# Performance work log

Measured on AMD Instinct MI355X. Metric: run time of the kernel, lower is better.

The kernel has to match this reference:

```python
import jax, jax.numpy as jnp
import numpy as np

N = 30000      # num nodes (cells)
E = 480000     # num edges (avg degree 16)
D_IN = 1000    # input_dim (genes)
H = 8          # nheads
F_H = 32       # hidden_dim per head
D_EMB = 64     # embedding_dim
NEG_SLOPE = 0.2


def setup_inputs() -> dict:
    key = jax.random.key(0)
    ks = jax.random.split(key, 12)
    glorot = lambda k, shape, fan: (jax.random.normal(k, shape, jnp.float32)
                                    * (1.0 / np.sqrt(fan)))
    return {
        "x": jax.random.normal(ks[0], (N, D_IN), jnp.float32),
        "edge_index": jax.random.randint(ks[1], (2, E), 0, N),
        "edge_weight": jax.random.uniform(ks[2], (E,), jnp.float32),
        # GATConv params
        "W": glorot(ks[3], (D_IN, H * F_H), D_IN),
        "att_src": glorot(ks[4], (H, F_H), F_H),
        "att_dst": glorot(ks[5], (H, F_H), F_H),
        "bias_gat": jnp.zeros((H * F_H,), jnp.float32),
        # embedding Linear
        "emb_W": glorot(ks[6], (H * F_H, D_EMB), H * F_H),
        "emb_b": jnp.zeros((D_EMB,), jnp.float32),
        # decoder MLP
        "dec_W1": glorot(ks[7], (D_EMB, F_H), D_EMB),
        "dec_b1": jnp.zeros((F_H,), jnp.float32),
        "dec_W2": glorot(ks[8], (F_H, D_IN), F_H),
        "dec_b2": jnp.zeros((D_IN,), jnp.float32),
    }


def _gat_conv(x, edge_index, W, att_src, att_dst, bias):
    n = x.shape[0]
    h = (x @ W).reshape(n, H, F_H)                    # [N,H,F]
    a_s = jnp.einsum('nhf,hf->nh', h, att_src)        # [N,H]
    a_d = jnp.einsum('nhf,hf->nh', h, att_dst)        # [N,H]
    # add self loops (PyG default add_self_loops=True)
    loops = jnp.arange(n)
    src = jnp.concatenate([edge_index[0], loops])     # [E+N]
    dst = jnp.concatenate([edge_index[1], loops])     # [E+N]
    logits = jax.nn.leaky_relu(a_s[src] + a_d[dst], NEG_SLOPE)  # [E+N,H]
    # segment softmax over incoming edges of each destination node
    m = jax.ops.segment_max(logits, dst, num_segments=n)        # [N,H]
    p = jnp.exp(logits - m[dst])
    denom = jax.ops.segment_sum(p, dst, num_segments=n)         # [N,H]
    alpha = p / denom[dst]                                      # [E+N,H]
    msg = h[src] * alpha[:, :, None]                            # [E+N,H,F]
    out = jax.ops.segment_sum(msg, dst, num_segments=n)         # [N,H,F]
    return out.reshape(n, H * F_H) + bias


def reference(x, edge_index, edge_weight, W, att_src, att_dst, bias_gat,
              emb_W, emb_b, dec_W1, dec_b1, dec_W2, dec_b2):
    # edge_weight is accepted but unused: PyG GATConv with edge_dim=None has
    # no edge-feature pathway.
    h = jax.nn.relu(_gat_conv(x, edge_index, W, att_src, att_dst, bias_gat))
    z = h @ emb_W + emb_b                               # [N, D_EMB]
    d = jax.nn.relu(z @ dec_W1 + dec_b1)                # [N, F_H]
    recon = d @ dec_W2 + dec_b2                         # [N, D_IN]
    return recon, z
```

## Files before the change

kernel.cpp:

```cpp
#include <hip/hip_runtime.h>
#include <hip/hip_bf16.h>

#define N_NODES 30000
#define N_EDGES 480000
#define D_IN    1000
#define KPAD    1024
#define NHEAD   8
#define F_HID   32
#define D_EMB   64
#define NEG_SLOPE 0.2f
#define MAXDEG  64

typedef __attribute__((ext_vector_type(4))) float  f32x4;
typedef __attribute__((ext_vector_type(8))) __bf16 bf16x8;
typedef __attribute__((ext_vector_type(4))) __bf16 bf16x4;

#define WT_TOT    (256*KPAD + D_EMB*256 + F_HID*D_EMB + D_IN*F_HID)
#define WT_BLOCKS ((WT_TOT + 255) / 256)
#define WA_BLOCKS (16 * KPAD / 256)
#define SC_CHUNK  4068
#define SC_BLOCKS (118 * 8)

__global__ __launch_bounds__(256) void cvt_w(
    const float* __restrict__ W, const float* __restrict__ emb_W,
    const float* __restrict__ d1, const float* __restrict__ d2,
    const float* __restrict__ att_src, const float* __restrict__ att_dst,
    __bf16* __restrict__ WbT, __bf16* __restrict__ embT,
    __bf16* __restrict__ d1T, __bf16* __restrict__ d2T,
    __bf16* __restrict__ WaT,
    const int* __restrict__ eidx, int* __restrict__ cnt,
    int* __restrict__ slots)
{
    int b = blockIdx.x;
    if (b < WT_BLOCKS) {
        int i = b * 256 + threadIdx.x;
        if (i < 256 * KPAD) {
            int n = i >> 10, k = i & 1023;
            WbT[i] = (k < D_IN) ? (__bf16)W[(size_t)k * 256 + n] : (__bf16)0.0f;
            return;
        }
        i -= 256 * KPAD;
        if (i < D_EMB * 256) {
            int n = i >> 8, k = i & 255;
            embT[i] = (__bf16)emb_W[(size_t)k * D_EMB + n];
            return;
        }
        i -= D_EMB * 256;
        if (i < F_HID * D_EMB) {
            int n = i >> 6, k = i & 63;
            d1T[i] = (__bf16)d1[(size_t)k * F_HID + n];
            return;
        }
        i -= F_HID * D_EMB;
        if (i < D_IN * F_HID) {
            int n = i >> 5, k = i & 31;
            d2T[i] = (__bf16)d2[(size_t)k * D_IN + n];
        }
        return;
    }
    b -= WT_BLOCKS;
    if (b < WA_BLOCKS) {
        int i = b * 256 + threadIdx.x;
        int j = i >> 10, k = i & 1023;
        float s = 0.f;
        if (k < D_IN) {
            const float* av = (j < 8 ? att_src : att_dst) + (j & 7) * F_HID;
            const float* wr = W + (size_t)k * 256 + (j & 7) * F_HID;
            #pragma unroll
            for (int f = 0; f < F_HID; f++) s += wr[f] * av[f];
        }
        WaT[i] = (__bf16)s;
        return;
    }
    b -= WA_BLOCKS;
    {
        const int shard = blockIdx.x & 7;
        const int chunk = b >> 3;
        int e0 = chunk * SC_CHUNK;
        int e1 = e0 + SC_CHUNK; if (e1 > N_EDGES) e1 = N_EDGES;
        for (int e = e0 + (int)threadIdx.x; e < e1; e += 256) {
            int d = eidx[N_EDGES + e];
            if (((d >> 4) & 7) == shard) {
                int slot = atomicAdd(&cnt[d], 1);
                slots[d * MAXDEG + slot] = eidx[e];
            }
        }
    }
}

__device__ __forceinline__ void stage_tile(
    __bf16* lds, const __bf16* __restrict__ g, int base, int maxr,
    int K, int k0, int rows, int w, int lane, int stride)
{
    const int rsub = lane >> 2;
    const int c    = lane & 3;
    for (int off = w * 1024; off < rows * 64; off += stride) {
        int r  = (off >> 6) + rsub;
        int gr = base + r; gr = gr > maxr ? maxr : gr;
        int chunk = c ^ (r & 3);
        const __bf16* gp = g + (size_t)gr * K + k0 + chunk * 8;
        __builtin_amdgcn_global_load_lds(
            (const __attribute__((address_space(1))) void*)gp,
            (__attribute__((address_space(3))) void*)((char*)lds + off),
            16, 0, 0);
    }
}

#define GEMM1_BLOCKS ((N_NODES + 63) / 64)

__device__ __forceinline__ void xload8(const float* __restrict__ xrow, int cb,
                                       f32x4& u0, f32x4& u1)
{
    if (cb < D_IN) {
        const f32x4* p = (const f32x4*)(xrow + cb);
        u0 = p[0]; u1 = p[1];
    } else {
        u0 = (f32x4){0.f, 0.f, 0.f, 0.f};
        u1 = (f32x4){0.f, 0.f, 0.f, 0.f};
    }
}

__device__ __forceinline__ bf16x8 cvt8(const f32x4& u0, const f32x4& u1)
{
    bf16x8 o;
    o[0] = (__bf16)u0.x; o[1] = (__bf16)u0.y; o[2] = (__bf16)u0.z; o[3] = (__bf16)u0.w;
    o[4] = (__bf16)u1.x; o[5] = (__bf16)u1.y; o[6] = (__bf16)u1.z; o[7] = (__bf16)u1.w;
    return o;
}

__global__ __launch_bounds__(512, 4) void gemm1_fused(
    const float* __restrict__ x, const __bf16* __restrict__ WbT,
    const __bf16* __restrict__ WaT, __bf16* __restrict__ hb,
    float* __restrict__ a_s, float* __restrict__ a_d, int M)
{
    __shared__ __align__(16) __bf16 As[2][64 * 32];
    __shared__ __align__(16) __bf16 Bs[2][256 * 32];

    const int tid  = threadIdx.x;
    const int w    = tid >> 6, lane = tid & 63;
    const int wm   = w >> 2,   wn   = w & 3;
    const int quad = lane >> 4, l16 = lane & 15;
    const int bm   = blockIdx.x * 64;

    const bool astage = (tid < 256);
    const int r0   = tid >> 2;
    const int cpos = tid & 3;
    const int cxor = (cpos ^ (r0 & 3)) << 3;
    int grow = bm + r0; if (grow > M - 1) grow = M - 1;
    const float* xrow = x + (size_t)grow * D_IN;

    const int brsub = lane >> 2;
    const int bc    = lane & 3;

    f32x4 acc[2][4];
    #pragma unroll
    for (int i = 0; i < 2; i++)
        #pragma unroll
        for (int j = 0; j < 4; j++)
            acc[i][j] = (f32x4){0.f, 0.f, 0.f, 0.f};
    f32x4 accA[2];
    #pragma unroll
    for (int i = 0; i < 2; i++) accA[i] = (f32x4){0.f, 0.f, 0.f, 0.f};

    const bool att = (wn == 0);
    const __bf16* warow = WaT + (size_t)l16 * KPAD + quad * 8;

    auto stageB = [&](int buf, int k0) {
        #pragma unroll
        for (int off = 0; off < 16384; off += 8192) {
            int o2 = off + w * 1024;
            int r = (o2 >> 6) + brsub;
            int chunk = bc ^ (r & 3);
            const __bf16* gp = WbT + (size_t)r * KPAD + k0 + chunk * 8;
            __builtin_amdgcn_global_load_lds(
                (const __attribute__((address_space(1))) void*)gp,
                (__attribute__((address_space(3))) void*)((char*)&Bs[buf][0] + o2),
                16, 0, 0);
        }
    };

    auto compute = [&](int buf, const bf16x8& attfrag) {
        bf16x8 af[2], bfr[4];
        #pragma unroll
        for (int mt = 0; mt < 2; mt++) {
            int r = wm * 32 + mt * 16 + l16;
            af[mt] = *(const bf16x8*)&As[buf][r * 32 + (quad ^ (r & 3)) * 8];
        }
        #pragma unroll
        for (int nt = 0; nt < 4; nt++) {
            int r = wn * 64 + nt * 16 + l16;
            bfr[nt] = *(const bf16x8*)&Bs[buf][r * 32 + (quad ^ (r & 3)) * 8];
        }
        #pragma unroll
        for (int mt = 0; mt < 2; mt++)
            #pragma unroll
            for (int nt = 0; nt < 4; nt++)
                acc[mt][nt] = __builtin_amdgcn_mfma_f32_16x16x32_bf16(
                    af[mt], bfr[nt], acc[mt][nt], 0, 0, 0);
        if (att) {
            #pragma unroll
            for (int mt = 0; mt < 2; mt++)
                accA[mt] = __builtin_amdgcn_mfma_f32_16x16x32_bf16(
                    af[mt], attfrag, accA[mt], 0, 0, 0);
        }
    };

    f32x4 xa0, xa1, xb0, xb1;
    bf16x8 attEv = {}, attOd = {};

    if (astage) {
        xload8(xrow, 0 + cxor, xa0, xa1);
        xload8(xrow, 32 + cxor, xb0, xb1);
    }
    if (att) attEv = *(const bf16x8*)(warow + 0);
    if (astage) *(bf16x8*)&As[0][r0 * 32 + cpos * 8] = cvt8(xa0, xa1);
    stageB(0, 0);
    __syncthreads();

    for (int k0 = 0; k0 < KPAD; k0 += 64) {
        if (astage) {
            xload8(xrow, (k0 + 64) + cxor, xa0, xa1);
            *(bf16x8*)&As[1][r0 * 32 + cpos * 8] = cvt8(xb0, xb1);
        }
        if (att) attOd = *(const bf16x8*)(warow + k0 + 32);
        stageB(1, k0 + 32);
        compute(0, attEv);
        __syncthreads();

        if (k0 + 64 < KPAD) {
            if (astage) {
                xload8(xrow, (k0 + 96) + cxor, xb0, xb1);
                *(bf16x8*)&As[0][r0 * 32 + cpos * 8] = cvt8(xa0, xa1);
            }
            if (att) attEv = *(const bf16x8*)(warow + k0 + 64);
            stageB(0, k0 + 64);
        }
        compute(1, attOd);
        __syncthreads();
    }

    #pragma unroll
    for (int nt = 0; nt < 4; nt++) {
        int col = wn * 64 + nt * 16 + l16;
        #pragma unroll
        for (int mt = 0; mt < 2; mt++) {
            int row0 = bm + wm * 32 + mt * 16 + quad * 4;
            #pragma unroll
            for (int rr = 0; rr < 4; rr++) {
                int row = row0 + rr;
                if (row < M)
                    hb[(size_t)row * 256 + col] = (__bf16)acc[mt][nt][rr];
            }
        }
    }
    if (att) {
        #pragma unroll
        for (int mt = 0; mt < 2; mt++) {
            int row0 = bm + wm * 32 + mt * 16 + quad * 4;
            #pragma unroll
            for (int rr = 0; rr < 4; rr++) {
                int row = row0 + rr;
                if (row < M) {
                    float v = accA[mt][rr];
                    if (l16 < 8) a_s[row * NHEAD + l16] = v;
                    else         a_d[row * NHEAD + (l16 - 8)] = v;
                }
            }
        }
    }
}

__device__ __forceinline__ float leaky(float x) {
    return x > 0.f ? x : NEG_SLOPE * x;
}

__global__ __launch_bounds__(256) void gat_aggregate(
    const __bf16* __restrict__ hb, const float* __restrict__ a_s,
    const float* __restrict__ a_d, const int* __restrict__ cnt,
    const int* __restrict__ slots, const float* __restrict__ bias,
    __bf16* __restrict__ hgatb)
{
    const int wid  = threadIdx.x >> 6;
    const int lane = threadIdx.x & 63;
    const int n = blockIdx.x * 4 + wid;
    if (n >= N_NODES) return;

    const int hh = lane >> 3;
    const int fo = (lane & 7) * 4;
    const int base = n * MAXDEG;
    const int c = cnt[n];
    const float adn = a_d[n * NHEAD + hh];

    float p = __expf(leaky(a_s[n * NHEAD + hh] + adn));
    float denom = p;
    f32x4 acc;
    {
        bf16x4 hv = *(const bf16x4*)(hb + (size_t)n * 256 + hh * F_HID + fo);
        acc.x = p * (float)hv[0]; acc.y = p * (float)hv[1];
        acc.z = p * (float)hv[2]; acc.w = p * (float)hv[3];
    }
    int e = 0;
    for (; e + 4 <= c; e += 4) {
        const int4 ss = *(const int4*)(slots + base + e);
        int s0 = ss.x, s1 = ss.y, s2 = ss.z, s3 = ss.w;
        float l0 = a_s[s0 * NHEAD + hh], l1 = a_s[s1 * NHEAD + hh];
        float l2 = a_s[s2 * NHEAD + hh], l3 = a_s[s3 * NHEAD + hh];
        bf16x4 h0 = *(const bf16x4*)(hb + (size_t)s0 * 256 + hh * F_HID + fo);
        bf16x4 h1 = *(const bf16x4*)(hb + (size_t)s1 * 256 + hh * F_HID + fo);
        bf16x4 h2 = *(const bf16x4*)(hb + (size_t)s2 * 256 + hh * F_HID + fo);
        bf16x4 h3 = *(const bf16x4*)(hb + (size_t)s3 * 256 + hh * F_HID + fo);
        float p0 = __expf(leaky(l0 + adn)), p1 = __expf(leaky(l1 + adn));
        float p2 = __expf(leaky(l2 + adn)), p3 = __expf(leaky(l3 + adn));
        denom += (p0 + p1) + (p2 + p3);
        acc.x += p0*(float)h0[0] + p1*(float)h1[0] + p2*(float)h2[0] + p3*(float)h3[0];
        acc.y += p0*(float)h0[1] + p1*(float)h1[1] + p2*(float)h2[1] + p3*(float)h3[1];
        acc.z += p0*(float)h0[2] + p1*(float)h1[2] + p2*(float)h2[2] + p3*(float)h3[2];
        acc.w += p0*(float)h0[3] + p1*(float)h1[3] + p2*(float)h2[3] + p3*(float)h3[3];
    }
    for (; e < c; e++) {
        int s = slots[base + e];
        float pe = __expf(leaky(a_s[s * NHEAD + hh] + adn));
        denom += pe;
        bf16x4 hv = *(const bf16x4*)(hb + (size_t)s * 256 + hh * F_HID + fo);
        acc.x += pe * (float)hv[0]; acc.y += pe * (float)hv[1];
        acc.z += pe * (float)hv[2]; acc.w += pe * (float)hv[3];
    }
    float inv = 1.0f / denom;
    f32x4 bv = *(const f32x4*)(bias + lane * 4);
    float o0 = acc.x * inv + bv.x, o1 = acc.y * inv + bv.y;
    float o2 = acc.z * inv + bv.z, o3 = acc.w * inv + bv.w;
    o0 = o0 > 0.f ? o0 : 0.f;
    o1 = o1 > 0.f ? o1 : 0.f;
    o2 = o2 > 0.f ? o2 : 0.f;
    o3 = o3 > 0.f ? o3 : 0.f;
    bf16x4 ob;
    ob[0] = (__bf16)o0; ob[1] = (__bf16)o1; ob[2] = (__bf16)o2; ob[3] = (__bf16)o3;
    *(bf16x4*)(hgatb + (size_t)n * 256 + lane * 4) = ob;
}

__global__ __launch_bounds__(256) void gemm_zdr(
    const __bf16* __restrict__ hgatb, const __bf16* __restrict__ embT,
    const __bf16* __restrict__ d1T, const __bf16* __restrict__ d2T,
    const float* __restrict__ emb_b, const float* __restrict__ dec_b1,
    const float* __restrict__ dec_b2, float* __restrict__ z,
    float* __restrict__ recon, int M)
{
    __shared__ __align__(16) __bf16 smem[10240];
    __bf16* As  = smem;
    __bf16* Bs  = smem + 2048;
    __bf16* zS  = smem + 4096;
    __bf16* Bs2 = smem + 8192;

    const int tid  = threadIdx.x;
    const int w    = tid >> 6, lane = tid & 63;
    const int wm   = w >> 1,   wn   = w & 1;
    const int quad = lane >> 4, l16 = lane & 15;
    const int bm = blockIdx.x * 64;

    stage_tile(Bs2,        d1T, 0, 31, 64, 0,  32, w, lane, 4096);
    stage_tile(Bs2 + 1024, d1T, 0, 31, 64, 32, 32, w, lane, 4096);

    f32x4 acc[2][2];
    #pragma unroll
    for (int i = 0; i < 2; i++) { acc[i][0] = (f32x4){0,0,0,0}; acc[i][1] = (f32x4){0,0,0,0}; }

    for (int k0 = 0; k0 < 256; k0 += 32) {
        stage_tile(As, hgatb, bm, M - 1, 256, k0, 64, w, lane, 4096);
        stage_tile(Bs, embT,  0,  D_EMB - 1, 256, k0, 64, w, lane, 4096);
        __syncthreads();
        bf16x8 af[2], bfr[2];
        #pragma unroll
        for (int mt = 0; mt < 2; mt++) {
            int r = wm * 32 + mt * 16 + l16;
            af[mt] = *(const bf16x8*)&As[r * 32 + (quad ^ (r & 3)) * 8];
        }
        #pragma unroll
        for (int nt = 0; nt < 2; nt++) {
            int r = wn * 32 + nt * 16 + l16;
            bfr[nt] = *(const bf16x8*)&Bs[r * 32 + (quad ^ (r & 3)) * 8];
        }
        #pragma unroll
        for (int mt = 0; mt < 2; mt++)
            #pragma unroll
            for (int nt = 0; nt < 2; nt++)
                acc[mt][nt] = __builtin_amdgcn_mfma_f32_16x16x32_bf16(
                    af[mt], bfr[nt], acc[mt][nt], 0, 0, 0);
        __syncthreads();
    }

    #pragma unroll
    for (int nt = 0; nt < 2; nt++) {
        int col = wn * 32 + nt * 16 + l16;
        float bv = emb_b[col];
        int t = col >> 5, cch = (col >> 3) & 3, j = col & 7;
        #pragma unroll
        for (int mt = 0; mt < 2; mt++) {
            int rl0 = wm * 32 + mt * 16 + quad * 4;
            #pragma unroll
            for (int rr = 0; rr < 4; rr++) {
                int rl = rl0 + rr;
                int row = bm + rl;
                float v = acc[mt][nt][rr] + bv;
                if (row < M) z[(size_t)row * D_EMB + col] = v;
                zS[t * 2048 + rl * 32 + (cch ^ (rl & 3)) * 8 + j] = (__bf16)v;
            }
        }
    }
    __syncthreads();

    f32x4 accd[2];
    accd[0] = (f32x4){0,0,0,0}; accd[1] = (f32x4){0,0,0,0};
    #pragma unroll
    for (int t = 0; t < 2; t++) {
        bf16x8 af[2], bfr;
        #pragma unroll
        for (int mt = 0; mt < 2; mt++) {
            int r = wm * 32 + mt * 16 + l16;
            af[mt] = *(const bf16x8*)&zS[t * 2048 + r * 32 + (quad ^ (r & 3)) * 8];
        }
        {
            int r = wn * 16 + l16;
            bfr = *(const bf16x8*)&Bs2[t * 1024 + r * 32 + (quad ^ (r & 3)) * 8];
        }
        #pragma unroll
        for (int mt = 0; mt < 2; mt++)
            accd[mt] = __builtin_amdgcn_mfma_f32_16x16x32_bf16(af[mt], bfr, accd[mt], 0, 0, 0);
    }
    {
        int col = wn * 16 + l16;
        float bv = dec_b1[col];
        int cc = col >> 3, j = col & 7;
        #pragma unroll
        for (int mt = 0; mt < 2; mt++) {
            int rl0 = wm * 32 + mt * 16 + quad * 4;
            #pragma unroll
            for (int rr = 0; rr < 4; rr++) {
                int rl = rl0 + rr;
                float v = accd[mt][rr] + bv;
                v = v > 0.f ? v : 0.f;
                As[rl * 32 + (cc ^ (rl & 3)) * 8 + j] = (__bf16)v;
            }
        }
    }
    __syncthreads();

    bf16x8 daf[2];
    #pragma unroll
    for (int mt = 0; mt < 2; mt++) {
        int r = wm * 32 + mt * 16 + l16;
        daf[mt] = *(const bf16x8*)&As[r * 32 + (quad ^ (r & 3)) * 8];
    }
    for (int tt = wn; tt < 63; tt += 2) {
        int crow = tt * 16 + l16;
        if (crow > D_IN - 1) crow = D_IN - 1;
        bf16x8 bfr = *(const bf16x8*)&d2T[(size_t)crow * 32 + quad * 8];
        f32x4 a[2];
        #pragma unroll
        for (int mt = 0; mt < 2; mt++) {
            a[mt] = (f32x4){0.f, 0.f, 0.f, 0.f};
            a[mt] = __builtin_amdgcn_mfma_f32_16x16x32_bf16(bfr, daf[mt], a[mt], 0, 0, 0);
        }
        int col0 = tt * 16 + quad * 4;
        if (col0 + 3 < D_IN) {
            f32x4 bv = *(const f32x4*)&dec_b2[col0];
            #pragma unroll
            for (int mt = 0; mt < 2; mt++) {
                int row = bm + wm * 32 + mt * 16 + l16;
                if (row < M) {
                    f32x4 o;
                    o.x = a[mt].x + bv.x; o.y = a[mt].y + bv.y;
                    o.z = a[mt].z + bv.z; o.w = a[mt].w + bv.w;
                    *(f32x4*)&recon[(size_t)row * D_IN + col0] = o;
                }
            }
        }
    }
}

extern "C" void kernel_launch(void* const* d_in, const int* in_sizes, int n_in,
                              void* d_out, int out_size, void* d_ws, size_t ws_size,
                              hipStream_t stream)
{
    const float* x        = (const float*)d_in[0];
    const int*   eidx     = (const int*)  d_in[1];
    const float* W        = (const float*)d_in[3];
    const float* att_src  = (const float*)d_in[4];
    const float* att_dst  = (const float*)d_in[5];
    const float* bias_gat = (const float*)d_in[6];
    const float* emb_W    = (const float*)d_in[7];
    const float* emb_b    = (const float*)d_in[8];
    const float* dec_W1   = (const float*)d_in[9];
    const float* dec_b1   = (const float*)d_in[10];
    const float* dec_W2   = (const float*)d_in[11];
    const float* dec_b2   = (const float*)d_in[12];

    float* out   = (float*)d_out;
    float* recon = out;
    float* z     = out + (size_t)N_NODES * D_IN;

    char* ws = (char*)d_ws;
    size_t o = 0;
    auto alloc = [&](size_t bytes) { char* p = ws + o; o = (o + bytes + 255) & ~(size_t)255; return p; };
    __bf16* hb      = (__bf16*)alloc((size_t)N_NODES * 256 * 2);
    __bf16* WbT     = (__bf16*)alloc((size_t)256 * KPAD * 2);
    __bf16* embT    = (__bf16*)alloc((size_t)D_EMB * 256 * 2);
    __bf16* d1T     = (__bf16*)alloc((size_t)F_HID * D_EMB * 2);
    __bf16* d2T     = (__bf16*)alloc((size_t)D_IN * F_HID * 2);
    __bf16* WaT     = (__bf16*)alloc((size_t)16 * KPAD * 2);
    __bf16* hgatb   = (__bf16*)alloc((size_t)N_NODES * 256 * 2);
    float*  a_s     = (float*) alloc((size_t)N_NODES * NHEAD * 4);
    float*  a_d     = (float*) alloc((size_t)N_NODES * NHEAD * 4);
    int*    slots   = (int*)   alloc((size_t)N_NODES * MAXDEG * 4);
    int*    cnt     = (int*)   alloc((size_t)N_NODES * 4);

    hipMemsetAsync(cnt, 0, (size_t)N_NODES * 4, stream);

    cvt_w<<<WT_BLOCKS + WA_BLOCKS + SC_BLOCKS, 256, 0, stream>>>(
        W, emb_W, dec_W1, dec_W2, att_src, att_dst,
        WbT, embT, d1T, d2T, WaT, eidx, cnt, slots);

    gemm1_fused<<<GEMM1_BLOCKS, 512, 0, stream>>>(
        x, WbT, WaT, hb, a_s, a_d, N_NODES);

    gat_aggregate<<<N_NODES / 4, 256, 0, stream>>>(
        hb, a_s, a_d, cnt, slots, bias_gat, hgatb);

    gemm_zdr<<<(N_NODES + 63) / 64, 256, 0, stream>>>(
        hgatb, embT, d1T, d2T, emb_b, dec_b1, dec_b2, z, recon, N_NODES);
}
```

Before: 376.1 us.

## Drop LDS staging in gemm1; load W fragments directly from global per wave

Rewrites the first GEMM so each wave owns 16 rows and all 256 output columns. A and B fragments are loaded straight from global memory into registers, so the LDS double-buffering and barriers are gone. The aim is to remove shared-memory traffic and synchronisation overhead. In exchange every wave re-reads the full W matrix from global/L2 with no reuse across waves, and the 16 accumulators plus 16 B fragments raise register pressure.

```diff
diff --git a/kernel.cpp b/kernel.cpp
--- a/kernel.cpp
+++ b/kernel.cpp
@@ -108,18 +108,6 @@
 
 #define GEMM1_BLOCKS ((N_NODES + 63) / 64)
 
-__device__ __forceinline__ void xload8(const float* __restrict__ xrow, int cb,
-                                       f32x4& u0, f32x4& u1)
-{
-    if (cb < D_IN) {
-        const f32x4* p = (const f32x4*)(xrow + cb);
-        u0 = p[0]; u1 = p[1];
-    } else {
-        u0 = (f32x4){0.f, 0.f, 0.f, 0.f};
-        u1 = (f32x4){0.f, 0.f, 0.f, 0.f};
-    }
-}
-
 __device__ __forceinline__ bf16x8 cvt8(const f32x4& u0, const f32x4& u1)
 {
     bf16x8 o;
@@ -128,144 +116,75 @@
     return o;
 }
 
-__global__ __launch_bounds__(512, 4) void gemm1_fused(
+__global__ __launch_bounds__(256) void gemm1_fused(
     const float* __restrict__ x, const __bf16* __restrict__ WbT,
     const __bf16* __restrict__ WaT, __bf16* __restrict__ hb,
     float* __restrict__ a_s, float* __restrict__ a_d, int M)
 {
-    __shared__ __align__(16) __bf16 As[2][64 * 32];
-    __shared__ __align__(16) __bf16 Bs[2][256 * 32];
-
     const int tid  = threadIdx.x;
-    const int w    = tid >> 6, lane = tid & 63;
-    const int wm   = w >> 2,   wn   = w & 3;
+    const int wv   = tid >> 6, lane = tid & 63;
     const int quad = lane >> 4, l16 = lane & 15;
     const int bm   = blockIdx.x * 64;
 
-    const bool astage = (tid < 256);
-    const int r0   = tid >> 2;
-    const int cpos = tid & 3;
-    const int cxor = (cpos ^ (r0 & 3)) << 3;
-    int grow = bm + r0; if (grow > M - 1) grow = M - 1;
-    const float* xrow = x + (size_t)grow * D_IN;
-
-    const int brsub = lane >> 2;
-    const int bc    = lane & 3;
-
-    f32x4 acc[2][4];
-    #pragma unroll
-    for (int i = 0; i < 2; i++)
-        #pragma unroll
-        for (int j = 0; j < 4; j++)
-            acc[i][j] = (f32x4){0.f, 0.f, 0.f, 0.f};
-    f32x4 accA[2];
-    #pragma unroll
-    for (int i = 0; i < 2; i++) accA[i] = (f32x4){0.f, 0.f, 0.f, 0.f};
-
-    const bool att = (wn == 0);
-    const __bf16* warow = WaT + (size_t)l16 * KPAD + quad * 8;
-
-    auto stageB = [&](int buf, int k0) {
-        #pragma unroll
-        for (int off = 0; off < 16384; off += 8192) {
-            int o2 = off + w * 1024;
-            int r = (o2 >> 6) + brsub;
-            int chunk = bc ^ (r & 3);
-            const __bf16* gp = WbT + (size_t)r * KPAD + k0 + chunk * 8;
-            __builtin_amdgcn_global_load_lds(
-                (const __attribute__((address_space(1))) void*)gp,
-                (__attribute__((address_space(3))) void*)((char*)&Bs[buf][0] + o2),
-                16, 0, 0);
+    int arow = bm + wv * 16 + l16; if (arow > M - 1) arow = M - 1;
+    const float* xrow = x + (size_t)arow * D_IN;
+    const int koff = quad * 8;
+
+    f32x4 acc[16];
+    #pragma unroll
+    for (int i = 0; i < 16; i++) acc[i] = (f32x4){0.f, 0.f, 0.f, 0.f};
+    f32x4 accA = (f32x4){0.f, 0.f, 0.f, 0.f};
+
+    const __bf16* wb   = WbT + (size_t)l16 * KPAD + koff;
+    const __bf16* wa   = WaT + (size_t)l16 * KPAD + koff;
+
+    auto loadx = [&](int k0, f32x4& u0, f32x4& u1) {
+        int kk = k0 + koff;
+        if (kk < D_IN) {
+            const f32x4* p = (const f32x4*)(xrow + kk);
+            u0 = p[0]; u1 = p[1];
+        } else {
+            u0 = (f32x4){0.f, 0.f, 0.f, 0.f};
+            u1 = (f32x4){0.f, 0.f, 0.f, 0.f};
         }
     };
 
-    auto compute = [&](int buf, const bf16x8& attfrag) {
-        bf16x8 af[2], bfr[4];
-        #pragma unroll
-        for (int mt = 0; mt < 2; mt++) {
-            int r = wm * 32 + mt * 16 + l16;
-            af[mt] = *(const bf16x8*)&As[buf][r * 32 + (quad ^ (r & 3)) * 8];
-        }
-        #pragma unroll
-        for (int nt = 0; nt < 4; nt++) {
-            int r = wn * 64 + nt * 16 + l16;
-            bfr[nt] = *(const bf16x8*)&Bs[buf][r * 32 + (quad ^ (r & 3)) * 8];
-        }
-        #pragma unroll
-        for (int mt = 0; mt < 2; mt++)
-            #pragma unroll
-            for (int nt = 0; nt < 4; nt++)
-                acc[mt][nt] = __builtin_amdgcn_mfma_f32_16x16x32_bf16(
-                    af[mt], bfr[nt], acc[mt][nt], 0, 0, 0);
-        if (att) {
-            #pragma unroll
-            for (int mt = 0; mt < 2; mt++)
-                accA[mt] = __builtin_amdgcn_mfma_f32_16x16x32_bf16(
-                    af[mt], attfrag, accA[mt], 0, 0, 0);
-        }
-    };
-
-    f32x4 xa0, xa1, xb0, xb1;
-    bf16x8 attEv = {}, attOd = {};
-
-    if (astage) {
-        xload8(xrow, 0 + cxor, xa0, xa1);
-        xload8(xrow, 32 + cxor, xb0, xb1);
-    }
-    if (att) attEv = *(const bf16x8*)(warow + 0);
-    if (astage) *(bf16x8*)&As[0][r0 * 32 + cpos * 8] = cvt8(xa0, xa1);
-    stageB(0, 0);
-    __syncthreads();
-
-    for (int k0 = 0; k0 < KPAD; k0 += 64) {
-        if (astage) {
-            xload8(xrow, (k0 + 64) + cxor, xa0, xa1);
-            *(bf16x8*)&As[1][r0 * 32 + cpos * 8] = cvt8(xb0, xb1);
-        }
-        if (att) attOd = *(const bf16x8*)(warow + k0 + 32);
-        stageB(1, k0 + 32);
-        compute(0, attEv);
-        __syncthreads();
-
-        if (k0 + 64 < KPAD) {
-            if (astage) {
-                xload8(xrow, (k0 + 96) + cxor, xb0, xb1);
-                *(bf16x8*)&As[0][r0 * 32 + cpos * 8] = cvt8(xa0, xa1);
-            }
-            if (att) attEv = *(const bf16x8*)(warow + k0 + 64);
-            stageB(0, k0 + 64);
-        }
-        compute(1, attOd);
-        __syncthreads();
-    }
-
-    #pragma unroll
-    for (int nt = 0; nt < 4; nt++) {
-        int col = wn * 64 + nt * 16 + l16;
-        #pragma unroll
-        for (int mt = 0; mt < 2; mt++) {
-            int row0 = bm + wm * 32 + mt * 16 + quad * 4;
-            #pragma unroll
-            for (int rr = 0; rr < 4; rr++) {
-                int row = row0 + rr;
-                if (row < M)
-                    hb[(size_t)row * 256 + col] = (__bf16)acc[mt][nt][rr];
-            }
-        }
-    }
-    if (att) {
-        #pragma unroll
-        for (int mt = 0; mt < 2; mt++) {
-            int row0 = bm + wm * 32 + mt * 16 + quad * 4;
-            #pragma unroll
-            for (int rr = 0; rr < 4; rr++) {
-                int row = row0 + rr;
-                if (row < M) {
-                    float v = accA[mt][rr];
-                    if (l16 < 8) a_s[row * NHEAD + l16] = v;
-                    else         a_d[row * NHEAD + (l16 - 8)] = v;
-                }
-            }
+    f32x4 xc0, xc1, xn0, xn1;
+    loadx(0, xc0, xc1);
+
+    for (int k0 = 0; k0 < KPAD; k0 += 32) {
+        loadx(k0 + 32, xn0, xn1);
+        bf16x8 bfr[16];
+        #pragma unroll
+        for (int nt = 0; nt < 16; nt++)
+            bfr[nt] = *(const bf16x8*)(wb + (size_t)nt * 16 * KPAD + k0);
+        bf16x8 attf = *(const bf16x8*)(wa + k0);
+        bf16x8 af = cvt8(xc0, xc1);
+        #pragma unroll
+        for (int nt = 0; nt < 16; nt++)
+            acc[nt] = __builtin_amdgcn_mfma_f32_16x16x32_bf16(af, bfr[nt], acc[nt], 0, 0, 0);
+        accA = __builtin_amdgcn_mfma_f32_16x16x32_bf16(af, attf, accA, 0, 0, 0);
+        xc0 = xn0; xc1 = xn1;
+    }
+
+    const int row0 = bm + wv * 16 + quad * 4;
+    #pragma unroll
+    for (int nt = 0; nt < 16; nt++) {
+        int col = nt * 16 + l16;
+        #pragma unroll
+        for (int rr = 0; rr < 4; rr++) {
+            int row = row0 + rr;
+            if (row < M)
+                hb[(size_t)row * 256 + col] = (__bf16)acc[nt][rr];
+        }
+    }
+    #pragma unroll
+    for (int rr = 0; rr < 4; rr++) {
+        int row = row0 + rr;
+        if (row < M) {
+            float v = accA[rr];
+            if (l16 < 8) a_s[row * NHEAD + l16] = v;
+            else         a_d[row * NHEAD + (l16 - 8)] = v;
         }
     }
 }
@@ -519,7 +438,7 @@
         W, emb_W, dec_W1, dec_W2, att_src, att_dst,
         WbT, embT, d1T, d2T, WaT, eidx, cnt, slots);
 
-    gemm1_fused<<<GEMM1_BLOCKS, 512, 0, stream>>>(
+    gemm1_fused<<<GEMM1_BLOCKS, 256, 0, stream>>>(
         x, WbT, WaT, hb, a_s, a_d, N_NODES);
 
     gat_aggregate<<<N_NODES / 4, 256, 0, stream>>>(
```

Measured after the change: 457.9 us. 21.7% more time.

## Shrink GEMM1 block to four waves each computing a full 64x64 tile

Applied to the files above, without the earlier changes.

The main x@W GEMM kernel moves from 512 threads (8 waves, 2x4 wave grid, 32x64 per wave) to 256 threads (4 waves, each 64 rows by 64 cols). Every thread now stages A, which removes the idle half of threads during x loading, and B staging goes through a shared stage_tile helper. Each wave reuses more of its A and B fragments per MFMA, but it holds twice as many accumulators, which raises register pressure and may lower occupancy and latency hiding. The attention-logit MFMA path now runs only on wave 0, covering four m-tiles.

```diff
diff --git a/kernel.cpp b/kernel.cpp
--- a/kernel.cpp
+++ b/kernel.cpp
@@ -128,7 +128,7 @@
     return o;
 }
 
-__global__ __launch_bounds__(512, 4) void gemm1_fused(
+__global__ __launch_bounds__(256, 2) void gemm1_fused(
     const float* __restrict__ x, const __bf16* __restrict__ WbT,
     const __bf16* __restrict__ WaT, __bf16* __restrict__ hb,
     float* __restrict__ a_s, float* __restrict__ a_d, int M)
@@ -137,69 +137,54 @@
     __shared__ __align__(16) __bf16 Bs[2][256 * 32];
 
     const int tid  = threadIdx.x;
-    const int w    = tid >> 6, lane = tid & 63;
-    const int wm   = w >> 2,   wn   = w & 3;
+    const int wv   = tid >> 6, lane = tid & 63;
     const int quad = lane >> 4, l16 = lane & 15;
     const int bm   = blockIdx.x * 64;
 
-    const bool astage = (tid < 256);
     const int r0   = tid >> 2;
     const int cpos = tid & 3;
     const int cxor = (cpos ^ (r0 & 3)) << 3;
     int grow = bm + r0; if (grow > M - 1) grow = M - 1;
     const float* xrow = x + (size_t)grow * D_IN;
 
-    const int brsub = lane >> 2;
-    const int bc    = lane & 3;
-
-    f32x4 acc[2][4];
-    #pragma unroll
-    for (int i = 0; i < 2; i++)
+    f32x4 acc[4][4];
+    #pragma unroll
+    for (int i = 0; i < 4; i++)
         #pragma unroll
         for (int j = 0; j < 4; j++)
             acc[i][j] = (f32x4){0.f, 0.f, 0.f, 0.f};
-    f32x4 accA[2];
-    #pragma unroll
-    for (int i = 0; i < 2; i++) accA[i] = (f32x4){0.f, 0.f, 0.f, 0.f};
-
-    const bool att = (wn == 0);
+    f32x4 accA[4];
+    #pragma unroll
+    for (int i = 0; i < 4; i++) accA[i] = (f32x4){0.f, 0.f, 0.f, 0.f};
+
+    const bool att = (wv == 0);
     const __bf16* warow = WaT + (size_t)l16 * KPAD + quad * 8;
 
     auto stageB = [&](int buf, int k0) {
-        #pragma unroll
-        for (int off = 0; off < 16384; off += 8192) {
-            int o2 = off + w * 1024;
-            int r = (o2 >> 6) + brsub;
-            int chunk = bc ^ (r & 3);
-            const __bf16* gp = WbT + (size_t)r * KPAD + k0 + chunk * 8;
-            __builtin_amdgcn_global_load_lds(
-                (const __attribute__((address_space(1))) void*)gp,
-                (__attribute__((address_space(3))) void*)((char*)&Bs[buf][0] + o2),
-                16, 0, 0);
-        }
+        stage_tile(&Bs[buf][0], WbT, 0, 255, KPAD, k0, 256, wv, lane, 4096);
     };
 
     auto compute = [&](int buf, const bf16x8& attfrag) {
-        bf16x8 af[2], bfr[4];
-        #pragma unroll
-        for (int mt = 0; mt < 2; mt++) {
-            int r = wm * 32 + mt * 16 + l16;
+        bf16x8 af[4], bfr[4];
+        #pragma unroll
+        for (int mt = 0; mt < 4; mt++) {
+            int r = mt * 16 + l16;
             af[mt] = *(const bf16x8*)&As[buf][r * 32 + (quad ^ (r & 3)) * 8];
         }
         #pragma unroll
         for (int nt = 0; nt < 4; nt++) {
-            int r = wn * 64 + nt * 16 + l16;
+            int r = wv * 64 + nt * 16 + l16;
             bfr[nt] = *(const bf16x8*)&Bs[buf][r * 32 + (quad ^ (r & 3)) * 8];
         }
         #pragma unroll
-        for (int mt = 0; mt < 2; mt++)
+        for (int mt = 0; mt < 4; mt++)
             #pragma unroll
             for (int nt = 0; nt < 4; nt++)
                 acc[mt][nt] = __builtin_amdgcn_mfma_f32_16x16x32_bf16(
                     af[mt], bfr[nt], acc[mt][nt], 0, 0, 0);
         if (att) {
             #pragma unroll
-            for (int mt = 0; mt < 2; mt++)
+            for (int mt = 0; mt < 4; mt++)
                 accA[mt] = __builtin_amdgcn_mfma_f32_16x16x32_bf16(
                     af[mt], attfrag, accA[mt], 0, 0, 0);
         }
@@ -208,30 +193,24 @@
     f32x4 xa0, xa1, xb0, xb1;
     bf16x8 attEv = {}, attOd = {};
 
-    if (astage) {
-        xload8(xrow, 0 + cxor, xa0, xa1);
-        xload8(xrow, 32 + cxor, xb0, xb1);
-    }
+    xload8(xrow, 0 + cxor, xa0, xa1);
+    xload8(xrow, 32 + cxor, xb0, xb1);
     if (att) attEv = *(const bf16x8*)(warow + 0);
-    if (astage) *(bf16x8*)&As[0][r0 * 32 + cpos * 8] = cvt8(xa0, xa1);
+    *(bf16x8*)&As[0][r0 * 32 + cpos * 8] = cvt8(xa0, xa1);
     stageB(0, 0);
     __syncthreads();
 
     for (int k0 = 0; k0 < KPAD; k0 += 64) {
-        if (astage) {
-            xload8(xrow, (k0 + 64) + cxor, xa0, xa1);
-            *(bf16x8*)&As[1][r0 * 32 + cpos * 8] = cvt8(xb0, xb1);
-        }
+        xload8(xrow, (k0 + 64) + cxor, xa0, xa1);
+        *(bf16x8*)&As[1][r0 * 32 + cpos * 8] = cvt8(xb0, xb1);
         if (att) attOd = *(const bf16x8*)(warow + k0 + 32);
         stageB(1, k0 + 32);
         compute(0, attEv);
         __syncthreads();
 
         if (k0 + 64 < KPAD) {
-            if (astage) {
-                xload8(xrow, (k0 + 96) + cxor, xb0, xb1);
-                *(bf16x8*)&As[0][r0 * 32 + cpos * 8] = cvt8(xa0, xa1);
-            }
+            xload8(xrow, (k0 + 96) + cxor, xb0, xb1);
+            *(bf16x8*)&As[0][r0 * 32 + cpos * 8] = cvt8(xa0, xa1);
             if (att) attEv = *(const bf16x8*)(warow + k0 + 64);
             stageB(0, k0 + 64);
         }
@@ -241,10 +220,10 @@
 
     #pragma unroll
     for (int nt = 0; nt < 4; nt++) {
-        int col = wn * 64 + nt * 16 + l16;
-        #pragma unroll
-        for (int mt = 0; mt < 2; mt++) {
-            int row0 = bm + wm * 32 + mt * 16 + quad * 4;
+        int col = wv * 64 + nt * 16 + l16;
+        #pragma unroll
+        for (int mt = 0; mt < 4; mt++) {
+            int row0 = bm + mt * 16 + quad * 4;
             #pragma unroll
             for (int rr = 0; rr < 4; rr++) {
                 int row = row0 + rr;
@@ -255,8 +234,8 @@
     }
     if (att) {
         #pragma unroll
-        for (int mt = 0; mt < 2; mt++) {
-            int row0 = bm + wm * 32 + mt * 16 + quad * 4;
+        for (int mt = 0; mt < 4; mt++) {
+            int row0 = bm + mt * 16 + quad * 4;
             #pragma unroll
             for (int rr = 0; rr < 4; rr++) {
                 int row = row0 + rr;
@@ -519,7 +498,7 @@
         W, emb_W, dec_W1, dec_W2, att_src, att_dst,
         WbT, embT, d1T, d2T, WaT, eidx, cnt, slots);
 
-    gemm1_fused<<<GEMM1_BLOCKS, 512, 0, stream>>>(
+    gemm1_fused<<<GEMM1_BLOCKS, 256, 0, stream>>>(
         x, WbT, WaT, hb, a_s, a_d, N_NODES);
 
     gat_aggregate<<<N_NODES / 4, 256, 0, stream>>>(
```

Result: no change. 379.2 us (+0.8%).

## Fuse GAT aggregation into the embedding/decoder GEMM kernel via shared memory

Applied to the files above, without the earlier changes.

Merges the neighbor aggregation kernel with the z/decoder GEMM kernel: each 512-thread block aggregates 64 nodes directly into a padded shared-memory tile, then runs the embedding, decoder and reconstruction MFMAs from it. This removes the global hgatb intermediate round trip and one kernel launch. In exchange the gather phase runs with far fewer, larger blocks and more shared memory per block, which may reduce latency hiding for the irregular neighbor loads, and the work split across 8 waves changes.

```diff
diff --git a/kernel.cpp b/kernel.cpp
--- a/kernel.cpp
+++ b/kernel.cpp
@@ -270,127 +270,120 @@
     }
 }
 
+#define HROW 264
+
 __device__ __forceinline__ float leaky(float x) {
     return x > 0.f ? x : NEG_SLOPE * x;
 }
 
-__global__ __launch_bounds__(256) void gat_aggregate(
+__global__ __launch_bounds__(512, 4) void gat_zdr(
     const __bf16* __restrict__ hb, const float* __restrict__ a_s,
     const float* __restrict__ a_d, const int* __restrict__ cnt,
     const int* __restrict__ slots, const float* __restrict__ bias,
-    __bf16* __restrict__ hgatb)
-{
-    const int wid  = threadIdx.x >> 6;
-    const int lane = threadIdx.x & 63;
-    const int n = blockIdx.x * 4 + wid;
-    if (n >= N_NODES) return;
-
-    const int hh = lane >> 3;
-    const int fo = (lane & 7) * 4;
-    const int base = n * MAXDEG;
-    const int c = cnt[n];
-    const float adn = a_d[n * NHEAD + hh];
-
-    float p = __expf(leaky(a_s[n * NHEAD + hh] + adn));
-    float denom = p;
-    f32x4 acc;
+    const __bf16* __restrict__ embT, const __bf16* __restrict__ d1T,
+    const __bf16* __restrict__ d2T, const float* __restrict__ emb_b,
+    const float* __restrict__ dec_b1, const float* __restrict__ dec_b2,
+    float* __restrict__ z, float* __restrict__ recon, int M)
+{
+    __shared__ __align__(16) __bf16 hgatS[64 * HROW];
+    __shared__ __align__(16) __bf16 Bs[64 * 32];
+    __shared__ __align__(16) __bf16 zS[64 * 64];
+    __shared__ __align__(16) __bf16 Bs2[2 * 32 * 32];
+    __shared__ __align__(16) __bf16 dS[64 * 32];
+
+    const int tid  = threadIdx.x;
+    const int wv   = tid >> 6, lane = tid & 63;
+    const int quad = lane >> 4, l16 = lane & 15;
+    const int bm   = blockIdx.x * 64;
+
+    stage_tile(Bs2,        d1T, 0, 31, 64, 0,  32, wv, lane, 4096);
+    stage_tile(Bs2 + 1024, d1T, 0, 31, 64, 32, 32, wv, lane, 4096);
+
     {
-        bf16x4 hv = *(const bf16x4*)(hb + (size_t)n * 256 + hh * F_HID + fo);
-        acc.x = p * (float)hv[0]; acc.y = p * (float)hv[1];
-        acc.z = p * (float)hv[2]; acc.w = p * (float)hv[3];
-    }
-    int e = 0;
-    for (; e + 4 <= c; e += 4) {
-        const int4 ss = *(const int4*)(slots + base + e);
-        int s0 = ss.x, s1 = ss.y, s2 = ss.z, s3 = ss.w;
-        float l0 = a_s[s0 * NHEAD + hh], l1 = a_s[s1 * NHEAD + hh];
-        float l2 = a_s[s2 * NHEAD + hh], l3 = a_s[s3 * NHEAD + hh];
-        bf16x4 h0 = *(const bf16x4*)(hb + (size_t)s0 * 256 + hh * F_HID + fo);
-        bf16x4 h1 = *(const bf16x4*)(hb + (size_t)s1 * 256 + hh * F_HID + fo);
-        bf16x4 h2 = *(const bf16x4*)(hb + (size_t)s2 * 256 + hh * F_HID + fo);
-        bf16x4 h3 = *(const bf16x4*)(hb + (size_t)s3 * 256 + hh * F_HID + fo);
-        float p0 = __expf(leaky(l0 + adn)), p1 = __expf(leaky(l1 + adn));
-        float p2 = __expf(leaky(l2 + adn)), p3 = __expf(leaky(l3 + adn));
-        denom += (p0 + p1) + (p2 + p3);
-        acc.x += p0*(float)h0[0] + p1*(float)h1[0] + p2*(float)h2[0] + p3*(float)h3[0];
-        acc.y += p0*(float)h0[1] + p1*(float)h1[1] + p2*(float)h2[1] + p3*(float)h3[1];
-        acc.z += p0*(float)h0[2] + p1*(float)h1[2] + p2*(float)h2[2] + p3*(float)h3[2];
-        acc.w += p0*(float)h0[3] + p1*(float)h1[3] + p2*(float)h2[3] + p3*(float)h3[3];
-    }
-    for (; e < c; e++) {
-        int s = slots[base + e];
-        float pe = __expf(leaky(a_s[s * NHEAD + hh] + adn));
-        denom += pe;
-        bf16x4 hv = *(const bf16x4*)(hb + (size_t)s * 256 + hh * F_HID + fo);
-        acc.x += pe * (float)hv[0]; acc.y += pe * (float)hv[1];
-        acc.z += pe * (float)hv[2]; acc.w += pe * (float)hv[3];
-    }
-    float inv = 1.0f / denom;
-    f32x4 bv = *(const f32x4*)(bias + lane * 4);
-    float o0 = acc.x * inv + bv.x, o1 = acc.y * inv + bv.y;
-    float o2 = acc.z * inv + bv.z, o3 = acc.w * inv + bv.w;
-    o0 = o0 > 0.f ? o0 : 0.f;
-    o1 = o1 > 0.f ? o1 : 0.f;
-    o2 = o2 > 0.f ? o2 : 0.f;
-    o3 = o3 > 0.f ? o3 : 0.f;
-    bf16x4 ob;
-    ob[0] = (__bf16)o0; ob[1] = (__bf16)o1; ob[2] = (__bf16)o2; ob[3] = (__bf16)o3;
-    *(bf16x4*)(hgatb + (size_t)n * 256 + lane * 4) = ob;
-}
-
-__global__ __launch_bounds__(256) void gemm_zdr(
-    const __bf16* __restrict__ hgatb, const __bf16* __restrict__ embT,
-    const __bf16* __restrict__ d1T, const __bf16* __restrict__ d2T,
-    const float* __restrict__ emb_b, const float* __restrict__ dec_b1,
-    const float* __restrict__ dec_b2, float* __restrict__ z,
-    float* __restrict__ recon, int M)
-{
-    __shared__ __align__(16) __bf16 smem[10240];
-    __bf16* As  = smem;
-    __bf16* Bs  = smem + 2048;
-    __bf16* zS  = smem + 4096;
-    __bf16* Bs2 = smem + 8192;
-
-    const int tid  = threadIdx.x;
-    const int w    = tid >> 6, lane = tid & 63;
-    const int wm   = w >> 1,   wn   = w & 1;
-    const int quad = lane >> 4, l16 = lane & 15;
-    const int bm = blockIdx.x * 64;
-
-    stage_tile(Bs2,        d1T, 0, 31, 64, 0,  32, w, lane, 4096);
-    stage_tile(Bs2 + 1024, d1T, 0, 31, 64, 32, 32, w, lane, 4096);
-
-    f32x4 acc[2][2];
-    #pragma unroll
-    for (int i = 0; i < 2; i++) { acc[i][0] = (f32x4){0,0,0,0}; acc[i][1] = (f32x4){0,0,0,0}; }
+        const int hh = lane >> 3;
+        const int fo = (lane & 7) * 4;
+        const f32x4 bv = *(const f32x4*)(bias + lane * 4);
+        for (int i = 0; i < 8; i++) {
+            int n = bm + wv * 8 + i;
+            if (n >= M) break;
+            const int base = n * MAXDEG;
+            const int c = cnt[n];
+            const float adn = a_d[n * NHEAD + hh];
+
+            float p = __expf(leaky(a_s[n * NHEAD + hh] + adn));
+            float denom = p;
+            f32x4 acc;
+            {
+                bf16x4 hv = *(const bf16x4*)(hb + (size_t)n * 256 + hh * F_HID + fo);
+                acc.x = p * (float)hv[0]; acc.y = p * (float)hv[1];
+                acc.z = p * (float)hv[2]; acc.w = p * (float)hv[3];
+            }
+            int e = 0;
+            for (; e + 4 <= c; e += 4) {
+                const int4 ss = *(const int4*)(slots + base + e);
+                int s0 = ss.x, s1 = ss.y, s2 = ss.z, s3 = ss.w;
+                float l0 = a_s[s0 * NHEAD + hh], l1 = a_s[s1 * NHEAD + hh];
+                float l2 = a_s[s2 * NHEAD + hh], l3 = a_s[s3 * NHEAD + hh];
+                bf16x4 h0 = *(const bf16x4*)(hb + (size_t)s0 * 256 + hh * F_HID + fo);
+                bf16x4 h1 = *(const bf16x4*)(hb + (size_t)s1 * 256 + hh * F_HID + fo);
+                bf16x4 h2 = *(const bf16x4*)(hb + (size_t)s2 * 256 + hh * F_HID + fo);
+                bf16x4 h3 = *(const bf16x4*)(hb + (size_t)s3 * 256 + hh * F_HID + fo);
+                float p0 = __expf(leaky(l0 + adn)), p1 = __expf(leaky(l1 + adn));
+                float p2 = __expf(leaky(l2 + adn)), p3 = __expf(leaky(l3 + adn));
+                denom += (p0 + p1) + (p2 + p3);
+                acc.x += p0*(float)h0[0] + p1*(float)h1[0] + p2*(float)h2[0] + p3*(float)h3[0];
+                acc.y += p0*(float)h0[1] + p1*(float)h1[1] + p2*(float)h2[1] + p3*(float)h3[1];
+                acc.z += p0*(float)h0[2] + p1*(float)h1[2] + p2*(float)h2[2] + p3*(float)h3[2];
+                acc.w += p0*(float)h0[3] + p1*(float)h1[3] + p2*(float)h2[3] + p3*(float)h3[3];
+            }
+            for (; e < c; e++) {
+                int s = slots[base + e];
+                float pe = __expf(leaky(a_s[s * NHEAD + hh] + adn));
+                denom += pe;
+                bf16x4 hv = *(const bf16x4*)(hb + (size_t)s * 256 + hh * F_HID + fo);
+                acc.x += pe * (float)hv[0]; acc.y += pe * (float)hv[1];
+                acc.z += pe * (float)hv[2]; acc.w += pe * (float)hv[3];
+            }
+            float inv = 1.0f / denom;
+            float o0 = acc.x * inv + bv.x, o1 = acc.y * inv + bv.y;
+            float o2 = acc.z * inv + bv.z, o3 = acc.w * inv + bv.w;
+            o0 = o0 > 0.f ? o0 : 0.f;
+            o1 = o1 > 0.f ? o1 : 0.f;
+            o2 = o2 > 0.f ? o2 : 0.f;
+            o3 = o3 > 0.f ? o3 : 0.f;
+            bf16x4 ob;
+            ob[0] = (__bf16)o0; ob[1] = (__bf16)o1; ob[2] = (__bf16)o2; ob[3] = (__bf16)o3;
+            *(bf16x4*)&hgatS[(wv * 8 + i) * HROW + lane * 4] = ob;
+        }
+    }
+    __syncthreads();
+
+    const int wm  = wv >> 2;
+    const int wn4 = wv & 3;
+    f32x4 acc[2];
+    acc[0] = (f32x4){0,0,0,0}; acc[1] = (f32x4){0,0,0,0};
 
     for (int k0 = 0; k0 < 256; k0 += 32) {
-        stage_tile(As, hgatb, bm, M - 1, 256, k0, 64, w, lane, 4096);
-        stage_tile(Bs, embT,  0,  D_EMB - 1, 256, k0, 64, w, lane, 4096);
+        stage_tile(Bs, embT, 0, D_EMB - 1, 256, k0, 64, wv, lane, 4096);
         __syncthreads();
-        bf16x8 af[2], bfr[2];
+        bf16x8 af[2], bfr;
         #pragma unroll
         for (int mt = 0; mt < 2; mt++) {
             int r = wm * 32 + mt * 16 + l16;
-            af[mt] = *(const bf16x8*)&As[r * 32 + (quad ^ (r & 3)) * 8];
-        }
-        #pragma unroll
-        for (int nt = 0; nt < 2; nt++) {
-            int r = wn * 32 + nt * 16 + l16;
-            bfr[nt] = *(const bf16x8*)&Bs[r * 32 + (quad ^ (r & 3)) * 8];
+            af[mt] = *(const bf16x8*)&hgatS[r * HROW + k0 + quad * 8];
+        }
+        {
+            int r = wn4 * 16 + l16;
+            bfr = *(const bf16x8*)&Bs[r * 32 + (quad ^ (r & 3)) * 8];
         }
         #pragma unroll
         for (int mt = 0; mt < 2; mt++)
-            #pragma unroll
-            for (int nt = 0; nt < 2; nt++)
-                acc[mt][nt] = __builtin_amdgcn_mfma_f32_16x16x32_bf16(
-                    af[mt], bfr[nt], acc[mt][nt], 0, 0, 0);
+            acc[mt] = __builtin_amdgcn_mfma_f32_16x16x32_bf16(af[mt], bfr, acc[mt], 0, 0, 0);
         __syncthreads();
     }
 
-    #pragma unroll
-    for (int nt = 0; nt < 2; nt++) {
-        int col = wn * 32 + nt * 16 + l16;
+    {
+        int col = wn4 * 16 + l16;
         float bv = emb_b[col];
         int t = col >> 5, cch = (col >> 3) & 3, j = col & 7;
         #pragma unroll
@@ -400,7 +393,7 @@
             for (int rr = 0; rr < 4; rr++) {
                 int rl = rl0 + rr;
                 int row = bm + rl;
-                float v = acc[mt][nt][rr] + bv;
+                float v = acc[mt][rr] + bv;
                 if (row < M) z[(size_t)row * D_EMB + col] = v;
                 zS[t * 2048 + rl * 32 + (cch ^ (rl & 3)) * 8 + j] = (__bf16)v;
             }
@@ -408,26 +401,26 @@
     }
     __syncthreads();
 
-    f32x4 accd[2];
-    accd[0] = (f32x4){0,0,0,0}; accd[1] = (f32x4){0,0,0,0};
-    #pragma unroll
-    for (int t = 0; t < 2; t++) {
-        bf16x8 af[2], bfr;
-        #pragma unroll
-        for (int mt = 0; mt < 2; mt++) {
-            int r = wm * 32 + mt * 16 + l16;
-            af[mt] = *(const bf16x8*)&zS[t * 2048 + r * 32 + (quad ^ (r & 3)) * 8];
-        }
-        {
-            int r = wn * 16 + l16;
-            bfr = *(const bf16x8*)&Bs2[t * 1024 + r * 32 + (quad ^ (r & 3)) * 8];
-        }
-        #pragma unroll
-        for (int mt = 0; mt < 2; mt++)
-            accd[mt] = __builtin_amdgcn_mfma_f32_16x16x32_bf16(af[mt], bfr, accd[mt], 0, 0, 0);
-    }
-    {
-        int col = wn * 16 + l16;
+    if (wn4 < 2) {
+        f32x4 accd[2];
+        accd[0] = (f32x4){0,0,0,0}; accd[1] = (f32x4){0,0,0,0};
+        #pragma unroll
+        for (int t = 0; t < 2; t++) {
+            bf16x8 af[2], bfr;
+            #pragma unroll
+            for (int mt = 0; mt < 2; mt++) {
+                int r = wm * 32 + mt * 16 + l16;
+                af[mt] = *(const bf16x8*)&zS[t * 2048 + r * 32 + (quad ^ (r & 3)) * 8];
+            }
+            {
+                int r = wn4 * 16 + l16;
+                bfr = *(const bf16x8*)&Bs2[t * 1024 + r * 32 + (quad ^ (r & 3)) * 8];
+            }
+            #pragma unroll
+            for (int mt = 0; mt < 2; mt++)
+                accd[mt] = __builtin_amdgcn_mfma_f32_16x16x32_bf16(af[mt], bfr, accd[mt], 0, 0, 0);
+        }
+        int col = wn4 * 16 + l16;
         float bv = dec_b1[col];
         int cc = col >> 3, j = col & 7;
         #pragma unroll
@@ -438,39 +431,42 @@
                 int rl = rl0 + rr;
                 float v = accd[mt][rr] + bv;
                 v = v > 0.f ? v : 0.f;
-                As[rl * 32 + (cc ^ (rl & 3)) * 8 + j] = (__bf16)v;
+                dS[rl * 32 + (cc ^ (rl & 3)) * 8 + j] = (__bf16)v;
             }
         }
     }
     __syncthreads();
 
-    bf16x8 daf[2];
-    #pragma unroll
-    for (int mt = 0; mt < 2; mt++) {
-        int r = wm * 32 + mt * 16 + l16;
-        daf[mt] = *(const bf16x8*)&As[r * 32 + (quad ^ (r & 3)) * 8];
-    }
-    for (int tt = wn; tt < 63; tt += 2) {
-        int crow = tt * 16 + l16;
-        if (crow > D_IN - 1) crow = D_IN - 1;
-        bf16x8 bfr = *(const bf16x8*)&d2T[(size_t)crow * 32 + quad * 8];
-        f32x4 a[2];
-        #pragma unroll
-        for (int mt = 0; mt < 2; mt++) {
-            a[mt] = (f32x4){0.f, 0.f, 0.f, 0.f};
-            a[mt] = __builtin_amdgcn_mfma_f32_16x16x32_bf16(bfr, daf[mt], a[mt], 0, 0, 0);
-        }
-        int col0 = tt * 16 + quad * 4;
-        if (col0 + 3 < D_IN) {
-            f32x4 bv = *(const f32x4*)&dec_b2[col0];
+    {
+        const int wtt = wv & 3;
+        bf16x8 daf[2];
+        #pragma unroll
+        for (int mt = 0; mt < 2; mt++) {
+            int r = wm * 32 + mt * 16 + l16;
+            daf[mt] = *(const bf16x8*)&dS[r * 32 + (quad ^ (r & 3)) * 8];
+        }
+        for (int tt = wtt; tt < 63; tt += 4) {
+            int crow = tt * 16 + l16;
+            if (crow > D_IN - 1) crow = D_IN - 1;
+            bf16x8 bfr = *(const bf16x8*)&d2T[(size_t)crow * 32 + quad * 8];
+            f32x4 a[2];
             #pragma unroll
             for (int mt = 0; mt < 2; mt++) {
-                int row = bm + wm * 32 + mt * 16 + l16;
-                if (row < M) {
-                    f32x4 o;
-                    o.x = a[mt].x + bv.x; o.y = a[mt].y + bv.y;
-                    o.z = a[mt].z + bv.z; o.w = a[mt].w + bv.w;
-                    *(f32x4*)&recon[(size_t)row * D_IN + col0] = o;
+                a[mt] = (f32x4){0.f, 0.f, 0.f, 0.f};
+                a[mt] = __builtin_amdgcn_mfma_f32_16x16x32_bf16(bfr, daf[mt], a[mt], 0, 0, 0);
+            }
+            int col0 = tt * 16 + quad * 4;
+            if (col0 + 3 < D_IN) {
+                f32x4 bv = *(const f32x4*)&dec_b2[col0];
+                #pragma unroll
+                for (int mt = 0; mt < 2; mt++) {
+                    int row = bm + wm * 32 + mt * 16 + l16;
+                    if (row < M) {
+                        f32x4 o;
+                        o.x = a[mt].x + bv.x; o.y = a[mt].y + bv.y;
+                        o.z = a[mt].z + bv.z; o.w = a[mt].w + bv.w;
+                        *(f32x4*)&recon[(size_t)row * D_IN + col0] = o;
+                    }
                 }
             }
         }
@@ -507,7 +503,6 @@
     __bf16* d1T     = (__bf16*)alloc((size_t)F_HID * D_EMB * 2);
     __bf16* d2T     = (__bf16*)alloc((size_t)D_IN * F_HID * 2);
     __bf16* WaT     = (__bf16*)alloc((size_t)16 * KPAD * 2);
-    __bf16* hgatb   = (__bf16*)alloc((size_t)N_NODES * 256 * 2);
     float*  a_s     = (float*) alloc((size_t)N_NODES * NHEAD * 4);
     float*  a_d     = (float*) alloc((size_t)N_NODES * NHEAD * 4);
     int*    slots   = (int*)   alloc((size_t)N_NODES * MAXDEG * 4);
@@ -522,9 +517,7 @@
     gemm1_fused<<<GEMM1_BLOCKS, 512, 0, stream>>>(
         x, WbT, WaT, hb, a_s, a_d, N_NODES);
 
-    gat_aggregate<<<N_NODES / 4, 256, 0, stream>>>(
-        hb, a_s, a_d, cnt, slots, bias_gat, hgatb);
-
-    gemm_zdr<<<(N_NODES + 63) / 64, 256, 0, stream>>>(
-        hgatb, embT, d1T, d2T, emb_b, dec_b1, dec_b2, z, recon, N_NODES);
-}
+    gat_zdr<<<GEMM1_BLOCKS, 512, 0, stream>>>(
+        hb, a_s, a_d, cnt, slots, bias_gat,
+        embT, d1T, d2T, emb_b, dec_b1, dec_b2, z, recon, N_NODES);
+}
```

After: 360.8 us. 1.04x faster.
